# Optimization experiments

Hardware: AMD Instinct MI355X
Metric: run time of the kernel (lower is better)

The kernel has to match this reference:

```python
import jax, jax.numpy as jnp
from jax import lax
import numpy as np

B, H, W = 128, 64, 64
L_I, L_H, L_Q, K = 3, 150, 16, 30
DN = ('NCHW', 'OIHW', 'NCHW')


def conv(x, w):
    return lax.conv_general_dilated(x, w, (1, 1), 'SAME', dimension_numbers=DN)


def setup_inputs() -> dict:
    key = jax.random.key(0)
    ks = jax.random.split(key, 10)
    return {
        'layout': jax.random.normal(ks[0], (B, 2, H, W), jnp.float32),
        'heatmap': jax.random.uniform(ks[1], (B, 1, H, W), jnp.float32),
        'h_w': jax.random.normal(ks[2], (L_H, L_I, 3, 3), jnp.float32) * 0.1,
        'h_b': jax.random.normal(ks[3], (L_H,), jnp.float32) * 0.1,
        'r_w': jax.random.normal(ks[4], (1, L_H, 1, 1), jnp.float32) * 0.1,
        'q_w': jax.random.normal(ks[5], (L_Q, 1, 3, 3), jnp.float32) * 0.1,
        'w': jax.random.normal(ks[6], (L_Q, 1, 3, 3), jnp.float32) * 0.1,
        'fc_w': jax.random.normal(ks[7], (4, L_Q), jnp.float32) * 0.1,
        'S1': jax.random.randint(ks[8], (B,), 0, H, jnp.int64),
        'S2': jax.random.randint(ks[9], (B,), 0, W, jnp.int64),
    }


def reference(layout, heatmap, h_w, h_b, r_w, q_w, w, fc_w, S1, S2):
    # X: [B, l_i, H, W]
    X = jnp.concatenate([layout, heatmap], axis=1)
    h = conv(X, h_w) + h_b[None, :, None, None]      # [B, l_h, H, W]
    r = conv(h, r_w)                                  # [B, 1, H, W]
    q = conv(r, q_w)                                  # [B, l_q, H, W]
    v = jnp.max(q, axis=1, keepdims=True)             # [B, 1, H, W]
    wq = jnp.concatenate([q_w, w], axis=1)            # [l_q, 2, 3, 3]

    def step(v, _):
        q = conv(jnp.concatenate([r, v], axis=1), wq)
        return jnp.max(q, axis=1, keepdims=True), None

    v, _ = lax.scan(step, v, None, length=K - 1)
    q = conv(jnp.concatenate([r, v], axis=1), wq)     # [B, l_q, H, W]

    b = jnp.arange(q.shape[0])
    q_out = q[b, :, S1, S2]                           # [B, l_q]
    logits = q_out @ fc_w.T                           # [B, 4]
    probs = jax.nn.softmax(logits, axis=-1)
    return logits, probs, v, r, heatmap
```

## Files before the change

kernel.cpp:

```cpp
#include <hip/hip_runtime.h>
#include <math.h>

#define NT 1024
#define PW 66
#define RR 52


template<int NIT, bool FIRST, bool LAST>
__global__ __launch_bounds__(NT, 4)
void vin_chunk(const float* __restrict__ layout,
               const float* __restrict__ heatmap,
               const float* __restrict__ h_w,
               const float* __restrict__ h_b,
               const float* __restrict__ r_w,
               const float* __restrict__ q_w,
               const float* __restrict__ w,
               const float* __restrict__ fc_w,
               const int* __restrict__ S1,
               const int* __restrict__ S2,
               float* __restrict__ vg,
               float* __restrict__ out)
{
    __shared__ float rh[28];
    __shared__ float r_s[RR * PW];
    __shared__ float va[RR * PW];
    __shared__ float vb[RR * PW];

    const int b2   = blockIdx.x;
    const int b    = b2 >> 1;
    const int half = b2 & 1;
    const int vlo  = half ? 16 : 0;
    const int tid  = threadIdx.x;

    for (int i = tid; i < RR * PW; i += NT) { r_s[i] = 0.f; va[i] = 0.f; vb[i] = 0.f; }
    __syncthreads();

    if (tid < 896) {
        const int coeff = tid >> 5, j = tid & 31;
        float s = 0.f;
        for (int c = j; c < 150; c += 32)
            s += r_w[c] * ((coeff < 27) ? h_w[c * 27 + coeff] : h_b[c]);
        s += __shfl_xor(s, 1, 32);  s += __shfl_xor(s, 2, 32);
        s += __shfl_xor(s, 4, 32);  s += __shfl_xor(s, 8, 32);
        s += __shfl_xor(s, 16, 32);
        if (j == 0) rh[coeff] = s;
    }
    const float* X0 = layout  + (size_t)b * 2 * 4096;
    const float* X1 = X0 + 4096;
    const float* X2 = heatmap + (size_t)b * 4096;
    for (int i = tid; i < RR * 64; i += NT) {
        const int M = i >> 6, col = i & 63;
        const int ir = vlo - 2 + M;
        if (ir >= 0 && ir < 64) {
            const int s = ir * 64 + col, d = M * PW + col + 1;
            r_s[d] = X0[s]; va[d] = X1[s]; vb[d] = X2[s];
        }
    }
    __syncthreads();

    float rv[4];
    int   rpx[4];
    #pragma unroll
    for (int k2 = 0; k2 < 4; ++k2) {
        const int i = tid + k2 * NT;
        rpx[k2] = -1;
        if (i < 50 * 64) {
            const int row = i >> 6, col = i & 63;
            float acc = rh[27];
            #pragma unroll
            for (int dy = 0; dy < 3; ++dy)
                #pragma unroll
                for (int dx = 0; dx < 3; ++dx) {
                    const int idx = (row + dy) * PW + col + dx;
                    acc = fmaf(rh[0 * 9 + dy * 3 + dx], r_s[idx], acc);
                    acc = fmaf(rh[1 * 9 + dy * 3 + dx], va[idx],  acc);
                    acc = fmaf(rh[2 * 9 + dy * 3 + dx], vb[idx],  acc);
                }
            const int ir = vlo - 1 + row;
            rv[k2]  = (ir >= 0 && ir < 64) ? acc : 0.f;
            rpx[k2] = row * PW + col + 1;
        }
    }
    __syncthreads();

    for (int i = tid; i < RR * PW; i += NT) { va[i] = 0.f; vb[i] = 0.f; }
    #pragma unroll
    for (int k2 = 0; k2 < 4; ++k2) if (rpx[k2] >= 0) r_s[rpx[k2]] = rv[k2];
    __syncthreads();

    const int wid  = tid >> 6, lane = tid & 63;
    const int g    = lane >> 4, p = lane & 15;
    const int c    = (wid & 3) * 16 + p;
    const int band = wid >> 2;
    const int rb0  = band * 12;

    if (!FIRST) {
        for (int i = tid; i < 48 * 64; i += NT) {
            const int L = (i >> 6) + 1, col = i & 63;
            va[L * PW + col + 1] = vg[b * 4096 + (vlo + L - 1) * 64 + col];
        }
    }

    float wq[36];
    #pragma unroll
    for (int t = 0; t < 36; ++t) wq[t] = q_w[g * 36 + t];

    float rq[48];
    {
        const float* rw = r_s + rb0 * PW + c;
        float a0[3], a1[3], a2[3];
        #pragma unroll
        for (int d = 0; d < 3; ++d) { a0[d] = rw[d]; a1[d] = rw[PW + d]; }
        #pragma unroll
        for (int j = 0; j < 12; ++j) {
            #pragma unroll
            for (int d = 0; d < 3; ++d) a2[d] = rw[(j + 2) * PW + d];
            #pragma unroll
            for (int cc = 0; cc < 4; ++cc) {
                float a = 0.f;
                #pragma unroll
                for (int d = 0; d < 3; ++d) {
                    a = fmaf(wq[cc * 9 + d],     a0[d], a);
                    a = fmaf(wq[cc * 9 + 3 + d], a1[d], a);
                    a = fmaf(wq[cc * 9 + 6 + d], a2[d], a);
                }
                rq[cc * 12 + j] = a;
            }
            if (FIRST) {
                float m = fmaxf(fmaxf(rq[0 * 12 + j], rq[1 * 12 + j]),
                                fmaxf(rq[2 * 12 + j], rq[3 * 12 + j]));
                m = fmaxf(m, __shfl_xor(m, 16));
                m = fmaxf(m, __shfl_xor(m, 32));
                if (g == 0) va[(1 + rb0 + j) * PW + c + 1] = m;
            }
            #pragma unroll
            for (int d = 0; d < 3; ++d) { a0[d] = a1[d]; a1[d] = a2[d]; }
        }
    }

    float wv[36];
    #pragma unroll
    for (int t = 0; t < 36; ++t) wv[t] = w[g * 36 + t];
    __syncthreads();

    float* vcur = va;
    float* vnxt = vb;
    #pragma unroll 1
    for (int it = 0; it < NIT; ++it) {
        const float* vw = vcur + rb0 * PW + c;
        float a0[3], a1[3], a2[3];
        #pragma unroll
        for (int d = 0; d < 3; ++d) { a0[d] = vw[d]; a1[d] = vw[PW + d]; }
        #pragma unroll
        for (int j = 0; j < 12; ++j) {
            #pragma unroll
            for (int d = 0; d < 3; ++d) a2[d] = vw[(j + 2) * PW + d];
            float q0 = rq[0 * 12 + j], q1 = rq[1 * 12 + j];
            float q2 = rq[2 * 12 + j], q3 = rq[3 * 12 + j];
            #pragma unroll
            for (int d = 0; d < 3; ++d) {
                q0 = fmaf(wv[0 + d],  a0[d], q0); q0 = fmaf(wv[3 + d],  a1[d], q0); q0 = fmaf(wv[6 + d],  a2[d], q0);
                q1 = fmaf(wv[9 + d],  a0[d], q1); q1 = fmaf(wv[12 + d], a1[d], q1); q1 = fmaf(wv[15 + d], a2[d], q1);
                q2 = fmaf(wv[18 + d], a0[d], q2); q2 = fmaf(wv[21 + d], a1[d], q2); q2 = fmaf(wv[24 + d], a2[d], q2);
                q3 = fmaf(wv[27 + d], a0[d], q3); q3 = fmaf(wv[30 + d], a1[d], q3); q3 = fmaf(wv[33 + d], a2[d], q3);
            }
            float m = fmaxf(fmaxf(q0, q1), fmaxf(q2, q3));
            m = fmaxf(m, __shfl_xor(m, 16));
            m = fmaxf(m, __shfl_xor(m, 32));
            if (g == 0) vnxt[(1 + rb0 + j) * PW + c + 1] = m;
            #pragma unroll
            for (int d = 0; d < 3; ++d) { a0[d] = a1[d]; a1[d] = a2[d]; }
        }
        __syncthreads();
        float* t = vcur; vcur = vnxt; vnxt = t;
    }

    if (!LAST) {
        for (int i = tid; i < 32 * 64; i += NT) {
            const int ir = half * 32 + (i >> 6), col = i & 63;
            vg[b * 4096 + ir * 64 + col] = vcur[(ir - vlo + 1) * PW + col + 1];
        }
    } else {
        float* out_v = out + 1024 + (size_t)b * 4096;
        for (int i = tid; i < 32 * 64; i += NT) {
            const int ir = half * 32 + (i >> 6), col = i & 63;
            out_v[ir * 64 + col] = vcur[(ir - vlo + 1) * PW + col + 1];
        }
    }
    if (FIRST) {
        float* out_r = out + 1024 + (size_t)128 * 4096 + (size_t)b * 4096;
        float* out_h = out + 1024 + (size_t)256 * 4096 + (size_t)b * 4096;
        for (int i = tid; i < 32 * 64; i += NT) {
            const int ir = half * 32 + (i >> 6), col = i & 63;
            out_r[ir * 64 + col] = r_s[(ir - vlo + 1) * PW + col + 1];
            out_h[ir * 64 + col] = X2[ir * 64 + col];
        }
    }

    if (LAST) {
        const int s1 = S1[b], s2 = S2[b];
        if ((s1 >> 5) == half && tid == 0) {
            float q16[16];
            #pragma unroll
            for (int o = 0; o < 16; ++o) {
                float acc = 0.f;
                #pragma unroll
                for (int dy = 0; dy < 3; ++dy)
                    #pragma unroll
                    for (int dx = 0; dx < 3; ++dx) {
                        const int li = (s1 + dy - vlo) * PW + s2 + dx;
                        acc = fmaf(q_w[o * 9 + dy * 3 + dx], r_s[li], acc);
                        acc = fmaf(w[o * 9 + dy * 3 + dx],  vcur[li], acc);
                    }
                q16[o] = acc;
            }
            float lg[4];
            #pragma unroll
            for (int j = 0; j < 4; ++j) {
                float a = 0.f;
                #pragma unroll
                for (int o = 0; o < 16; ++o) a = fmaf(fc_w[j * 16 + o], q16[o], a);
                lg[j] = a;
            }
            const float m  = fmaxf(fmaxf(lg[0], lg[1]), fmaxf(lg[2], lg[3]));
            const float e0 = expf(lg[0] - m), e1 = expf(lg[1] - m);
            const float e2 = expf(lg[2] - m), e3 = expf(lg[3] - m);
            const float s  = e0 + e1 + e2 + e3;
            out[b * 4 + 0] = lg[0]; out[b * 4 + 1] = lg[1];
            out[b * 4 + 2] = lg[2]; out[b * 4 + 3] = lg[3];
            out[512 + b * 4 + 0] = e0 / s; out[512 + b * 4 + 1] = e1 / s;
            out[512 + b * 4 + 2] = e2 / s; out[512 + b * 4 + 3] = e3 / s;
        }
    }
}

extern "C" void kernel_launch(void* const* d_in, const int* in_sizes, int n_in,
                              void* d_out, int out_size, void* d_ws, size_t ws_size,
                              hipStream_t stream) {
    const float* layout  = (const float*)d_in[0];
    const float* heatmap = (const float*)d_in[1];
    const float* h_w     = (const float*)d_in[2];
    const float* h_b     = (const float*)d_in[3];
    const float* r_w     = (const float*)d_in[4];
    const float* q_w     = (const float*)d_in[5];
    const float* w       = (const float*)d_in[6];
    const float* fc_w    = (const float*)d_in[7];
    const int*   S1      = (const int*)d_in[8];
    const int*   S2      = (const int*)d_in[9];
    float* out = (float*)d_out;
    float* vg  = (float*)d_ws;

    hipLaunchKernelGGL((vin_chunk<15, true,  false>), dim3(256), dim3(NT), 0, stream,
                       layout, heatmap, h_w, h_b, r_w, q_w, w, fc_w, S1, S2, vg, out);
    hipLaunchKernelGGL((vin_chunk<14, false, true>),  dim3(256), dim3(NT), 0, stream,
                       layout, heatmap, h_w, h_b, r_w, q_w, w, fc_w, S1, S2, vg, out);
}
```

Baseline: 116.7 us.

## Keep r-conv partials in AGPRs and use DPP quad max reduction

Changes the lane mapping so the four channel groups of one pixel sit in adjacent lanes. The cross-group max then uses two DPP quad permutes instead of ds_bpermute-based shuffles. The 48 precomputed r-conv partial sums move into accumulation registers through inline asm, freeing VGPRs under the 1024-thread launch bound. The cost is extra accvgpr read instructions in the inner loop. The new lane mapping also changes the LDS access pattern, which may add bank conflicts on the strided column reads.

```diff
diff --git a/kernel.cpp b/kernel.cpp
--- a/kernel.cpp
+++ b/kernel.cpp
@@ -5,6 +5,15 @@
 #define PW 66
 #define RR 52
 
+#define AW(arr, idx, val) asm("v_accvgpr_write_b32 %0, %1" : "=a"(arr[idx]) : "v"(val))
+#define AR(dst, arr, idx) asm("v_accvgpr_read_b32 %0, %1" : "=v"(dst) : "a"(arr[idx]))
+
+static __device__ __forceinline__ float quad_max(float m) {
+    int t = __builtin_amdgcn_update_dpp(__float_as_int(m), __float_as_int(m), 0xB1, 0xF, 0xF, false);
+    m = fmaxf(m, __int_as_float(t));
+    t = __builtin_amdgcn_update_dpp(__float_as_int(m), __float_as_int(m), 0x4E, 0xF, 0xF, false);
+    return fmaxf(m, __int_as_float(t));
+}
 
 template<int NIT, bool FIRST, bool LAST>
 __global__ __launch_bounds__(NT, 4)
@@ -89,7 +98,8 @@
     __syncthreads();
 
     const int wid  = tid >> 6, lane = tid & 63;
-    const int g    = lane >> 4, p = lane & 15;
+    const int g    = lane & 3;
+    const int p    = lane >> 2;
     const int c    = (wid & 3) * 16 + p;
     const int band = wid >> 2;
     const int rb0  = band * 12;
@@ -105,7 +115,7 @@
     #pragma unroll
     for (int t = 0; t < 36; ++t) wq[t] = q_w[g * 36 + t];
 
-    float rq[48];
+    float rqa[48];
     {
         const float* rw = r_s + rb0 * PW + c;
         float a0[3], a1[3], a2[3];
@@ -115,6 +125,7 @@
         for (int j = 0; j < 12; ++j) {
             #pragma unroll
             for (int d = 0; d < 3; ++d) a2[d] = rw[(j + 2) * PW + d];
+            float q4[4];
             #pragma unroll
             for (int cc = 0; cc < 4; ++cc) {
                 float a = 0.f;
@@ -124,13 +135,12 @@
                     a = fmaf(wq[cc * 9 + 3 + d], a1[d], a);
                     a = fmaf(wq[cc * 9 + 6 + d], a2[d], a);
                 }
-                rq[cc * 12 + j] = a;
+                q4[cc] = a;
+                AW(rqa, cc * 12 + j, a);
             }
             if (FIRST) {
-                float m = fmaxf(fmaxf(rq[0 * 12 + j], rq[1 * 12 + j]),
-                                fmaxf(rq[2 * 12 + j], rq[3 * 12 + j]));
-                m = fmaxf(m, __shfl_xor(m, 16));
-                m = fmaxf(m, __shfl_xor(m, 32));
+                float m = fmaxf(fmaxf(q4[0], q4[1]), fmaxf(q4[2], q4[3]));
+                m = quad_max(m);
                 if (g == 0) va[(1 + rb0 + j) * PW + c + 1] = m;
             }
             #pragma unroll
@@ -155,8 +165,11 @@
         for (int j = 0; j < 12; ++j) {
             #pragma unroll
             for (int d = 0; d < 3; ++d) a2[d] = vw[(j + 2) * PW + d];
-            float q0 = rq[0 * 12 + j], q1 = rq[1 * 12 + j];
-            float q2 = rq[2 * 12 + j], q3 = rq[3 * 12 + j];
+            float q0, q1, q2, q3;
+            AR(q0, rqa, 0 * 12 + j);
+            AR(q1, rqa, 1 * 12 + j);
+            AR(q2, rqa, 2 * 12 + j);
+            AR(q3, rqa, 3 * 12 + j);
             #pragma unroll
             for (int d = 0; d < 3; ++d) {
                 q0 = fmaf(wv[0 + d],  a0[d], q0); q0 = fmaf(wv[3 + d],  a1[d], q0); q0 = fmaf(wv[6 + d],  a2[d], q0);
@@ -165,8 +178,7 @@
                 q3 = fmaf(wv[27 + d], a0[d], q3); q3 = fmaf(wv[30 + d], a1[d], q3); q3 = fmaf(wv[33 + d], a2[d], q3);
             }
             float m = fmaxf(fmaxf(q0, q1), fmaxf(q2, q3));
-            m = fmaxf(m, __shfl_xor(m, 16));
-            m = fmaxf(m, __shfl_xor(m, 32));
+            m = quad_max(m);
             if (g == 0) vnxt[(1 + rb0 + j) * PW + c + 1] = m;
             #pragma unroll
             for (int d = 0; d < 3; ++d) { a0[d] = a1[d]; a1[d] = a2[d]; }
```

New measurement: 120.3 us. +3.1%, slower.
